# Kernel optimization log

Hardware: AMD Instinct MI355X
Metric: run time of the kernel (lower is better)

## Reference

```python
import jax, jax.numpy as jnp
import numpy as np

B = 2
M = 128
N = 128
D_EMBD = 512
N_HEADS = 8
D_HEAD = 64
S_WIN = 8
MW = M // S_WIN
NW = N // S_WIN
LEVELS = 3
S_REGION = [8, 6, 4]
S_POOL = [2, 2, 2]
THETA = 10000.0
POOLED = [(64, 64), (32, 32), (16, 16)]
RAD = THETA ** (-2.0 * jnp.arange(D_HEAD // 4, dtype=jnp.float32) / D_HEAD)


def rope(q, m_idx, n_idx):
    # 2D RoPE: first half of d_head rotated by row index, second half by col index
    m = m_idx.astype(jnp.float32)[:, None] * RAD  # (Lm, d_head//4)
    n = n_idx.astype(jnp.float32)[:, None] * RAD  # (Ln, d_head//4)
    cos_m, sin_m = jnp.cos(m)[:, None, :], jnp.sin(m)[:, None, :]
    cos_n, sin_n = jnp.cos(n)[None, :, :], jnp.sin(n)[None, :, :]
    d_half = D_HEAD // 2
    qm = q[..., :d_half].reshape(q.shape[:-1] + (d_half // 2, 2))
    qn = q[..., d_half:].reshape(q.shape[:-1] + (d_half // 2, 2))
    qm_rot = jnp.stack([cos_m * qm[..., 0] - sin_m * qm[..., 1],
                        sin_m * qm[..., 0] + cos_m * qm[..., 1]], axis=-1)
    qn_rot = jnp.stack([cos_n * qn[..., 0] - sin_n * qn[..., 1],
                        sin_n * qn[..., 0] + cos_n * qn[..., 1]], axis=-1)
    return jnp.concatenate([qm_rot.reshape(q.shape[:-1] + (d_half,)),
                            qn_rot.reshape(q.shape[:-1] + (d_half,))], axis=-1)


def extract_regions(X, cy, cx, k, pooled_mask):
    # X: (B,H,m,n,C), pooled_mask: (B,1,m,n,1). cy/cx mirror torch's in-place '+= pad'.
    b, h, m, n, c = X.shape
    pad = k // 2
    cy = cy + pad
    cx = cx + pad
    Xp = jnp.pad(X, ((0, 0), (0, 0), (pad, pad), (pad, pad), (0, 0)))
    mp = jnp.pad(pooled_mask, ((0, 0), (0, 0), (pad, pad), (pad, pad), (0, 0)))
    delta = jnp.arange(k) - k // 2
    YYg, XXg = jnp.meshgrid(cy, cx, indexing='ij')  # (Mw,Nw)
    YY = jnp.clip(YYg[..., None, None] + delta.reshape(1, 1, -1, 1), 0, m - 1)  # (Mw,Nw,k,1)
    XX = jnp.clip(XXg[..., None, None] + delta.reshape(1, 1, 1, -1), 0, n - 1)  # (Mw,Nw,1,k)
    regions = Xp[:, :, YY, XX, :]       # (B,H,Mw,Nw,k,k,C) broadcast gather
    mask_regions = mp[:, :, YY, XX, :]  # (B,1,Mw,Nw,k,k,1)
    mw, nw = YYg.shape
    regions = regions.transpose(0, 1, 2, 4, 3, 5, 6).reshape(b, h, mw * k, nw * k, c)
    mask_regions = mask_regions.reshape(mp.shape[0], 1, mw, nw, k * k, 1)
    return regions, mask_regions, YY - pad, XX - pad


def to_windows(x, s):
    # (B,h,Mw*s,Nw*s,d) -> (B,h,Mw,Nw,s*s,d)
    b, h, ms, ns, d = x.shape
    mw, nw = ms // s, ns // s
    return x.reshape(b, h, mw, s, nw, s, d).transpose(0, 1, 2, 4, 3, 5, 6).reshape(b, h, mw, nw, s * s, d)


def split_heads(x):
    b, m, n, _ = x.shape
    return x.reshape(b, m, n, N_HEADS, D_HEAD).transpose(0, 3, 1, 2, 4)


def forward(feature_map, pooled_map_0, pooled_map_1, pooled_map_2,
            pooled_mask_0, pooled_mask_1, pooled_mask_2,
            mask_q, freq_off, cy, cx, Wq, Wk, Wv, Wo):
    pooled_maps = [pooled_map_0, pooled_map_1, pooled_map_2]
    pooled_masks = [pooled_mask_0, pooled_mask_1, pooled_mask_2]
    Q = split_heads(feature_map @ Wq)           # (B,h,M,N,d)
    freq5 = freq_off[:, None]                   # (B,1,M,N,2*d_head)
    # query affine: M_grid/N_grid are identity arange gathers in the original code
    queries = Q * freq5[..., :D_HEAD] + freq5[..., D_HEAD:]
    queries = rope(queries, jnp.arange(M), jnp.arange(N))
    queries = to_windows(queries, S_WIN)        # (B,h,Mw,Nw,sw^2,d)
    mask_q5 = mask_q[:, None].astype(bool)      # (B,1,Mw,Nw,sw^2,1)

    K_list, V_list, maskK_list = [], [], []
    cy_run, cx_run = cy, cx
    for l in range(LEVELS):
        k = S_REGION[l]
        pad = k // 2
        Kl = split_heads(pooled_maps[l] @ Wk)
        Vl = split_heads(pooled_maps[l] @ Wv)
        pm5 = pooled_masks[l][:, None]          # (B,1,m,n,1)
        cy_run = cy_run // S_POOL[l]
        cx_run = cx_run // S_POOL[l]
        K_reg, mask_K, YY, XX = extract_regions(Kl, cy_run, cx_run, k, pm5)
        # torch extract_regions mutates cy/cx in place (+pad), so V sees shifted centers
        V_reg, _, _, _ = extract_regions(Vl, cy_run + pad, cx_run + pad, k, pm5)
        cy_run = cy_run + 2 * pad
        cx_run = cx_run + 2 * pad
        m_idx = jnp.clip(YY[:, 0, :, 0].reshape(-1) * S_POOL[l], 0, M - 1)  # (Mw*k,)
        n_idx = jnp.clip(XX[0, :, 0, :].reshape(-1) * S_POOL[l], 0, N - 1)  # (Nw*k,)
        fgl = freq5[:, :, m_idx[:, None], n_idx[None, :], :]  # (B,1,Mw*k,Nw*k,2d)
        K_reg = rope(K_reg * fgl[..., :D_HEAD] + fgl[..., D_HEAD:], m_idx, n_idx)
        V_reg = rope(V_reg * fgl[..., :D_HEAD] + fgl[..., D_HEAD:], m_idx, n_idx)
        K_list.append(to_windows(K_reg, k))
        V_list.append(to_windows(V_reg, k))
        maskK_list.append(mask_K)
    keys = jnp.concatenate(K_list, axis=-2)     # (B,h,Mw,Nw,S,d), S=sum(sr^2)=116
    vals = jnp.concatenate(V_list, axis=-2)
    mask_keys = jnp.concatenate(maskK_list, axis=-2)  # (B,1,Mw,Nw,S,1)
    attn_mask = mask_q5 & jnp.swapaxes(mask_keys, -1, -2).astype(bool)
    scores = jnp.einsum('bhmnqd,bhmnkd->bhmnqk', queries, keys) / jnp.sqrt(jnp.float32(D_HEAD))
    scores = jnp.where(attn_mask, scores, jnp.finfo(scores.dtype).min)
    att = jnp.einsum('bhmnqk,bhmnkd->bhmnqd', jax.nn.softmax(scores, axis=-1), vals)
    att = att.reshape(B, N_HEADS, MW, NW, S_WIN, S_WIN, D_HEAD)
    att = att.transpose(0, 2, 4, 3, 5, 1, 6).reshape(B, M, N, N_HEADS * D_HEAD)
    return att @ Wo


def setup_inputs():
    key = jax.random.key(0)
    ks = jax.random.split(key, 12)
    inp = {}
    inp['feature_map'] = jax.random.normal(ks[0], (B, M, N, D_EMBD), dtype=jnp.float32)
    for l in range(LEVELS):
        m, n = POOLED[l]
        inp['pooled_map_%d' % l] = jax.random.normal(ks[1 + l], (B, m, n, D_EMBD), dtype=jnp.float32)
        inp['pooled_mask_%d' % l] = jnp.ones((B, m, n, 1), dtype=jnp.float32)
    inp['mask_q'] = jnp.ones((B, MW, NW, S_WIN * S_WIN, 1), dtype=bool)
    inp['freq_off'] = jax.random.normal(ks[4], (B, M, N, 2 * D_HEAD), dtype=jnp.float32) * 0.1 + 1.0
    inp['cy'] = (jnp.arange(MW) * S_WIN + S_WIN // 2).astype(jnp.int32)
    inp['cx'] = (jnp.arange(NW) * S_WIN + S_WIN // 2).astype(jnp.int32)
    inp['Wq'] = jax.random.normal(ks[5], (D_EMBD, N_HEADS * D_HEAD), dtype=jnp.float32) / np.sqrt(D_EMBD)
    inp['Wk'] = jax.random.normal(ks[6], (D_EMBD, N_HEADS * D_HEAD), dtype=jnp.float32) / np.sqrt(D_EMBD)
    inp['Wv'] = jax.random.normal(ks[7], (D_EMBD, N_HEADS * D_HEAD), dtype=jnp.float32) / np.sqrt(D_EMBD)
    inp['Wo'] = jax.random.normal(ks[8], (N_HEADS * D_HEAD, D_EMBD), dtype=jnp.float32) / np.sqrt(N_HEADS * D_HEAD)
    return inp


def reference(feature_map, pooled_map_0, pooled_map_1, pooled_map_2,
              pooled_mask_0, pooled_mask_1, pooled_mask_2,
              mask_q, freq_off, cy, cx, Wq, Wk, Wv, Wo):
    return forward(feature_map, pooled_map_0, pooled_map_1, pooled_map_2,
                   pooled_mask_0, pooled_mask_1, pooled_mask_2,
                   mask_q, freq_off, cy, cx, Wq, Wk, Wv, Wo)
```

## Files before the change

### kernel.cpp

```cpp
#include <hip/hip_runtime.h>
#include <math.h>

#define BB 2
#define MM 128
#define NN 128
#define DE 512
#define NH 8
#define DH 64
#define SWIN 8
#define MWIN 16
#define NWIN 16
#define NKEY 116
#define NSLOT 128

#define NEG_MAX (-3.402823466e38f)
#define LN1E4_OVER_32 0.28782313662425575f

#define L0_BASE 0
#define L1_BASE 8192
#define L2_BASE 10240
#define NPOS_KV 10752

typedef __bf16 bf16_t;
typedef bf16_t bf16x8 __attribute__((ext_vector_type(8)));
typedef bf16_t bf16x4 __attribute__((ext_vector_type(4)));
typedef bf16_t bf16x2 __attribute__((ext_vector_type(2)));
typedef float  f32x4  __attribute__((ext_vector_type(4)));

#define CV_S0 16777216
#define CV_S1 20971520
#define CV_S2 22020096
#define CV_S3 22282240
#define CV_BLOCKS 21760
__global__ __launch_bounds__(256) void prep(
    const float* __restrict__ fmap, const float* __restrict__ p0,
    const float* __restrict__ p1, const float* __restrict__ p2,
    const float* __restrict__ Wq, const float* __restrict__ Wk,
    const float* __restrict__ Wv, const float* __restrict__ Wo,
    bf16_t* __restrict__ Afm, bf16_t* __restrict__ Ap0,
    bf16_t* __restrict__ Ap1, bf16_t* __restrict__ Ap2,
    bf16_t* __restrict__ Tq, bf16_t* __restrict__ Tk,
    bf16_t* __restrict__ Tv, bf16_t* __restrict__ To) {
    __shared__ float Ws[64][65];
    const int bid = blockIdx.x;
    const int tid = threadIdx.x;
    if (bid < CV_BLOCKS) {
        const int e = (bid * 256 + tid) * 4;
        const float* src; bf16_t* dst; int off;
        if (e < CV_S0)      { src = fmap; dst = Afm; off = e; }
        else if (e < CV_S1) { src = p0;   dst = Ap0; off = e - CV_S0; }
        else if (e < CV_S2) { src = p1;   dst = Ap1; off = e - CV_S1; }
        else if (e < CV_S3) { src = p2;   dst = Ap2; off = e - CV_S2; }
        else return;
        const float4 v = *(const float4*)(src + off);
        bf16x4 o;
        o[0] = (bf16_t)v.x; o[1] = (bf16_t)v.y; o[2] = (bf16_t)v.z; o[3] = (bf16_t)v.w;
        *(bf16x4*)(dst + off) = o;
    } else {
        const int idx = bid - CV_BLOCKS;
        const int w = idx >> 6, tile = idx & 63;
        const float* W = (w == 0) ? Wq : (w == 1) ? Wk : (w == 2) ? Wv : Wo;
        bf16_t*      T = (w == 0) ? Tq : (w == 1) ? Tk : (w == 2) ? Tv : To;
        const int tk0 = (tile >> 3) * 64;
        const int tn0 = (tile & 7) * 64;
#pragma unroll 4
        for (int i = 0; i < 16; ++i) {
            const int e = tid + i * 256;
            Ws[e >> 6][e & 63] = W[(tk0 + (e >> 6)) * 512 + tn0 + (e & 63)];
        }
        __syncthreads();
#pragma unroll 4
        for (int i = 0; i < 16; ++i) {
            const int e = tid + i * 256;
            const int ck = e & 63, rn = e >> 6;
            T[(size_t)(tn0 + rn) * 512 + tk0 + ck] = (bf16_t)Ws[ck][rn];
        }
    }
}

__device__ __forceinline__ void gemm_body(const bf16_t* __restrict__ A,
                                          const bf16_t* __restrict__ Bt,
                                          float* __restrict__ C,
                                          int row0, int col0) {
    __shared__ __align__(16) bf16_t sA[128][72];
    __shared__ __align__(16) bf16_t sB[128][72];
    const int tid  = threadIdx.x;
    const int wave = tid >> 6;
    const int lane = tid & 63;
    const int quad = lane >> 4;
    const int lr   = lane & 15;
    const int m_w  = (wave >> 1) * 64;
    const int n_w  = (wave & 1) * 64;

    f32x4 acc[4][4];
#pragma unroll
    for (int i = 0; i < 4; ++i)
#pragma unroll
        for (int j = 0; j < 4; ++j)
#pragma unroll
            for (int r = 0; r < 4; ++r) acc[i][j][r] = 0.0f;

    for (int k0 = 0; k0 < 512; k0 += 64) {
#pragma unroll
        for (int i = 0; i < 4; ++i) {
            const int c  = tid + i * 256;
            const int r  = c >> 3;
            const int cb = (c & 7) * 8;
            *(bf16x8*)&sA[r][cb] = *(const bf16x8*)(A  + (size_t)(row0 + r) * 512 + k0 + cb);
            *(bf16x8*)&sB[r][cb] = *(const bf16x8*)(Bt + (size_t)(col0 + r) * 512 + k0 + cb);
        }
        __syncthreads();
#pragma unroll
        for (int kk = 0; kk < 64; kk += 32) {
            bf16x8 af[4], bfr[4];
#pragma unroll
            for (int i = 0; i < 4; ++i)
                af[i] = *(const bf16x8*)&sA[m_w + i * 16 + lr][kk + quad * 8];
#pragma unroll
            for (int j = 0; j < 4; ++j)
                bfr[j] = *(const bf16x8*)&sB[n_w + j * 16 + lr][kk + quad * 8];
#pragma unroll
            for (int i = 0; i < 4; ++i)
#pragma unroll
                for (int j = 0; j < 4; ++j)
                    acc[i][j] = __builtin_amdgcn_mfma_f32_16x16x32_bf16(
                        af[i], bfr[j], acc[i][j], 0, 0, 0);
        }
        __syncthreads();
    }
#pragma unroll
    for (int i = 0; i < 4; ++i) {
        const int rb = row0 + m_w + i * 16 + quad * 4;
#pragma unroll
        for (int j = 0; j < 4; ++j) {
            const int col = col0 + n_w + j * 16 + lr;
#pragma unroll
            for (int r = 0; r < 4; ++r)
                C[(size_t)(rb + r) * 512 + col] = acc[i][j][r];
        }
    }
}

__global__ __launch_bounds__(256) void gemm_all(
    const bf16_t* __restrict__ Afm, const bf16_t* __restrict__ Ap0,
    const bf16_t* __restrict__ Ap1, const bf16_t* __restrict__ Ap2,
    const bf16_t* __restrict__ Tq, const bf16_t* __restrict__ Tk,
    const bf16_t* __restrict__ Tv,
    float* __restrict__ Qbuf, float* __restrict__ K0, float* __restrict__ V0,
    float* __restrict__ K1, float* __restrict__ V1,
    float* __restrict__ K2, float* __restrict__ V2) {
    const int t = blockIdx.x;
    const bf16_t* A; const bf16_t* Bt; float* C; int rt;
    if (t < 1024)      { A = Afm; Bt = Tq; C = Qbuf; rt = t >> 2; }
    else if (t < 1280) { A = Ap0; Bt = Tk; C = K0; rt = (t - 1024) >> 2; }
    else if (t < 1536) { A = Ap0; Bt = Tv; C = V0; rt = (t - 1280) >> 2; }
    else if (t < 1600) { A = Ap1; Bt = Tk; C = K1; rt = (t - 1536) >> 2; }
    else if (t < 1664) { A = Ap1; Bt = Tv; C = V1; rt = (t - 1600) >> 2; }
    else if (t < 1680) { A = Ap2; Bt = Tk; C = K2; rt = (t - 1664) >> 2; }
    else               { A = Ap2; Bt = Tv; C = V2; rt = (t - 1680) >> 2; }
    gemm_body(A, Bt, C, rt * 128, (t & 3) * 128);
}

__global__ __launch_bounds__(256) void gemm_out(const bf16_t* __restrict__ A,
                                                const bf16_t* __restrict__ Bt,
                                                float* __restrict__ C) {
    gemm_body(A, Bt, C, blockIdx.y * 128, blockIdx.x * 128);
}

__global__ __launch_bounds__(256) void rope_qb(const float* __restrict__ Q,
                                               const float* __restrict__ freq,
                                               bf16_t* __restrict__ Qb) {
    const int t   = blockIdx.x * 256 + threadIdx.x;
    const int pp  = t & 255;
    const int pos = t >> 8;
    const int n   = pos & 127;
    const int m   = (pos >> 7) & 127;
    const int h   = pp >> 5;
    const int pr  = pp & 31;
    const int p   = pr & 15;
    const int d0  = (pr < 16) ? (2 * p) : (32 + 2 * p);

    const float rad   = expf(-LN1E4_OVER_32 * (float)p);
    const float angle = (float)((pr < 16) ? m : n) * rad;
    float sn, cs;
    sincosf(angle, &sn, &cs);

    const size_t fb = (size_t)pos * 128;
    const size_t qb = (size_t)pos * 512 + h * 64;
    const float x0 = Q[qb + d0]     * freq[fb + d0]     + freq[fb + 64 + d0];
    const float x1 = Q[qb + d0 + 1] * freq[fb + d0 + 1] + freq[fb + 64 + d0 + 1];
    bf16x2 o;
    o[0] = (bf16_t)(cs * x0 - sn * x1);
    o[1] = (bf16_t)(sn * x0 + cs * x1);
    *(bf16x2*)(Qb + qb + d0) = o;
}

__global__ __launch_bounds__(256) void rope_kv(
    const float* __restrict__ K0, const float* __restrict__ K1, const float* __restrict__ K2,
    const float* __restrict__ V0, const float* __restrict__ V1, const float* __restrict__ V2,
    const float* __restrict__ freq,
    bf16_t* __restrict__ RK, bf16_t* __restrict__ RV) {
    const int pos = blockIdx.x;
    int l, ml, pad, rel;
    if (pos < L1_BASE)      { l = 0; ml = 64; pad = 4; rel = pos; }
    else if (pos < L2_BASE) { l = 1; ml = 32; pad = 3; rel = pos - L1_BASE; }
    else                    { l = 2; ml = 16; pad = 2; rel = pos - L2_BASE; }
    const int b  = rel / (ml * ml);
    const int yx = rel - b * ml * ml;
    const int y  = yx / ml, x = yx % ml;
    const int vy = min(y + pad, ml - 1 - pad);
    const int vx = min(x + pad, ml - 1 - pad);
    const int mi = min(2 * y, 127), ni = min(2 * x, 127);
    const float* Kl = (l == 0) ? K0 : (l == 1) ? K1 : K2;
    const float* Vl = (l == 0) ? V0 : (l == 1) ? V1 : V2;

    const int tid = threadIdx.x;
    const int h  = tid >> 5;
    const int pr = tid & 31;
    const int p  = pr & 15;
    const int d0 = (pr < 16) ? (2 * p) : (32 + 2 * p);
    const float rad = expf(-LN1E4_OVER_32 * (float)p);
    const float ang = (float)((pr < 16) ? mi : ni) * rad;
    float sn, cs;
    sincosf(ang, &sn, &cs);

    const size_t fb   = ((size_t)(b * 128 + mi) * 128 + ni) * 128;
    const float fs0 = freq[fb + d0],      fs1 = freq[fb + d0 + 1];
    const float fo0 = freq[fb + 64 + d0], fo1 = freq[fb + 64 + d0 + 1];
    const size_t kidx = ((size_t)(b * ml + y) * ml + x) * 512 + h * 64 + d0;
    const size_t vidx = ((size_t)(b * ml + vy) * ml + vx) * 512 + h * 64 + d0;
    const size_t oidx = (size_t)pos * 512 + h * 64 + d0;
    {
        const float x0 = Kl[kidx] * fs0 + fo0, x1 = Kl[kidx + 1] * fs1 + fo1;
        bf16x2 o;
        o[0] = (bf16_t)(cs * x0 - sn * x1);
        o[1] = (bf16_t)(sn * x0 + cs * x1);
        *(bf16x2*)(RK + oidx) = o;
    }
    {
        const float x0 = Vl[vidx] * fs0 + fo0, x1 = Vl[vidx + 1] * fs1 + fo1;
        bf16x2 o;
        o[0] = (bf16_t)(cs * x0 - sn * x1);
        o[1] = (bf16_t)(sn * x0 + cs * x1);
        *(bf16x2*)(RV + oidx) = o;
    }
}

#define SKS 72
#define SPS 136
#define SVS 134
__global__ __launch_bounds__(256, 4) void attn_mfma(
    const bf16_t* __restrict__ Qb,
    const bf16_t* __restrict__ RK, const bf16_t* __restrict__ RV,
    const float* __restrict__ pm0, const float* __restrict__ pm1, const float* __restrict__ pm2,
    const int* __restrict__ cy, const int* __restrict__ cx,
    bf16_t* __restrict__ att) {
    __shared__ __align__(16) bf16_t sK[NSLOT * SKS];
    __shared__ __align__(16) bf16_t sVt[64 * SVS];
    __shared__ int   sOff[NSLOT];
    __shared__ float sValid[NSLOT];
    bf16_t* sP = sK;

    const int tid = threadIdx.x;
    const int h  = blockIdx.x & 7;
    const int wx = (blockIdx.x >> 3) & 15;
    const int wy = (blockIdx.x >> 7) & 15;
    const int b  = blockIdx.x >> 11;

    const int wave = tid >> 6, lane = tid & 63, quad = lane >> 4, lr = lane & 15;

    const int qrow = wave * 16 + lr;
    const int mq0 = wy * 8 + (qrow >> 3), nq0 = wx * 8 + (qrow & 7);
    const bf16_t* qp = Qb + ((size_t)((b * 128 + mq0) * 128 + nq0)) * 512 + h * 64 + quad * 8;
    const bf16x8 af0 = *(const bf16x8*)qp;
    const bf16x8 af1 = *(const bf16x8*)(qp + 32);

    if (tid < NSLOT) {
        const int j = tid;
        int off = 0;
        bool valid = false;
        if (j < NKEY) {
            const int c0y = cy[wy] >> 1, c0x = cx[wx] >> 1;
            const int c1y = (c0y + 8) >> 1, c1x = (c0x + 8) >> 1;
            const int c2y = (c1y + 6) >> 1, c2x = (c1x + 6) >> 1;
            int dy, dx, cry, crx, ml, pad, lbase;
            if (j < 64)       { dy = j >> 3;           dx = j & 7;  cry = c0y; crx = c0x; ml = 64; pad = 4; lbase = L0_BASE; }
            else if (j < 100) { int u = j - 64;  dy = u / 6;  dx = u % 6; cry = c1y; crx = c1x; ml = 32; pad = 3; lbase = L1_BASE; }
            else              { int u = j - 100; dy = u >> 2; dx = u & 3; cry = c2y; crx = c2x; ml = 16; pad = 2; lbase = L2_BASE; }
            const int ky = min(cry + dy, ml - 1) - pad;
            const int kx = min(crx + dx, ml - 1) - pad;
            if (ky >= 0 && kx >= 0) {
                const float* pm = (j < 64) ? pm0 : (j < 100) ? pm1 : pm2;
                valid = (pm[(b * ml + ky) * ml + kx] != 0.0f);
            }
            off = (lbase + (b * ml + max(ky, 0)) * ml + max(kx, 0)) * 512 + h * 64;
        }
        sOff[tid]   = off;
        sValid[tid] = valid ? 1.0f : 0.0f;
    }
    __syncthreads();

#pragma unroll
    for (int it = 0; it < 4; ++it) {
        const int idx = tid + it * 256;
        const int j = idx >> 3, c = (idx & 7) * 8;
        const int off = sOff[j];
        *(bf16x8*)&sK[j * SKS + c] = *(const bf16x8*)(RK + off + c);
        const bf16x8 v = *(const bf16x8*)(RV + off + c);
#pragma unroll
        for (int e = 0; e < 8; ++e) sVt[(c + e) * SVS + j] = v[e];
    }
    __syncthreads();

    f32x4 accs[8];
#pragma unroll
    for (int nt = 0; nt < 8; ++nt)
#pragma unroll
        for (int r = 0; r < 4; ++r) accs[nt][r] = 0.0f;
#pragma unroll
    for (int nt = 0; nt < 8; ++nt) {
        const bf16x8 b0 = *(const bf16x8*)&sK[(nt * 16 + lr) * SKS + quad * 8];
        const bf16x8 b1 = *(const bf16x8*)&sK[(nt * 16 + lr) * SKS + quad * 8 + 32];
        accs[nt] = __builtin_amdgcn_mfma_f32_16x16x32_bf16(af0, b0, accs[nt], 0, 0, 0);
        accs[nt] = __builtin_amdgcn_mfma_f32_16x16x32_bf16(af1, b1, accs[nt], 0, 0, 0);
    }

    float P[8][4];
#pragma unroll
    for (int nt = 0; nt < 8; ++nt) {
        const float vf = sValid[nt * 16 + lr];
#pragma unroll
        for (int r = 0; r < 4; ++r)
            P[nt][r] = (vf != 0.0f) ? accs[nt][r] * 0.125f : NEG_MAX;
    }

#pragma unroll
    for (int r = 0; r < 4; ++r) {
        float mx = P[0][r];
#pragma unroll
        for (int nt = 1; nt < 8; ++nt) mx = fmaxf(mx, P[nt][r]);
        for (int m = 1; m < 16; m <<= 1) mx = fmaxf(mx, __shfl_xor(mx, m));
        float sum = 0.0f;
#pragma unroll
        for (int nt = 0; nt < 8; ++nt) {
            const float e = __expf(P[nt][r] - mx);
            P[nt][r] = e;
            sum += e;
        }
        for (int m = 1; m < 16; m <<= 1) sum += __shfl_xor(sum, m);
        const float inv = 1.0f / sum;
#pragma unroll
        for (int nt = 0; nt < 8; ++nt) P[nt][r] *= inv;
    }

    __syncthreads();

#pragma unroll
    for (int nt = 0; nt < 8; ++nt)
#pragma unroll
        for (int r = 0; r < 4; ++r)
            sP[(wave * 16 + quad * 4 + r) * SPS + nt * 16 + lr] = (bf16_t)P[nt][r];
    __syncthreads();

    f32x4 acco[4];
#pragma unroll
    for (int nt = 0; nt < 4; ++nt)
#pragma unroll
        for (int r = 0; r < 4; ++r) acco[nt][r] = 0.0f;

    bf16x8 pa[4];
#pragma unroll
    for (int ks = 0; ks < 4; ++ks)
        pa[ks] = *(const bf16x8*)&sP[(wave * 16 + lr) * SPS + quad * 8 + ks * 32];
#pragma unroll
    for (int nt = 0; nt < 4; ++nt) {
#pragma unroll
        for (int ks = 0; ks < 4; ++ks) {
            const bf16x8 vb = *(const bf16x8*)&sVt[(nt * 16 + lr) * SVS + quad * 8 + ks * 32];
            acco[nt] = __builtin_amdgcn_mfma_f32_16x16x32_bf16(pa[ks], vb, acco[nt], 0, 0, 0);
        }
    }

#pragma unroll
    for (int nt = 0; nt < 4; ++nt) {
#pragma unroll
        for (int r = 0; r < 4; ++r) {
            const int q  = wave * 16 + quad * 4 + r;
            const int d  = nt * 16 + lr;
            const int mq = wy * 8 + (q >> 3), nq = wx * 8 + (q & 7);
            att[((size_t)((b * 128 + mq) * 128 + nq)) * 512 + h * 64 + d] = (bf16_t)acco[nt][r];
        }
    }
}

extern "C" void kernel_launch(void* const* d_in, const int* in_sizes, int n_in,
                              void* d_out, int out_size, void* d_ws, size_t ws_size,
                              hipStream_t stream) {
    const float* fmap = (const float*)d_in[0];
    const float* p0   = (const float*)d_in[1];
    const float* pm0  = (const float*)d_in[2];
    const float* p1   = (const float*)d_in[3];
    const float* pm1  = (const float*)d_in[4];
    const float* p2   = (const float*)d_in[5];
    const float* pm2  = (const float*)d_in[6];
    const float* freq = (const float*)d_in[8];
    const int*   cy   = (const int*)d_in[9];
    const int*   cx   = (const int*)d_in[10];
    const float* Wq   = (const float*)d_in[11];
    const float* Wk   = (const float*)d_in[12];
    const float* Wv   = (const float*)d_in[13];
    const float* Wo   = (const float*)d_in[14];
    float* out = (float*)d_out;

    char* base = (char*)d_ws;
    size_t off = 0;
    auto carve = [&](size_t bytes) {
        char* p = base + off; off += (bytes + 255) & ~(size_t)255; return p;
    };
    float*  Qbuf = (float*)carve(67108864);
    float*  K0   = (float*)carve(16777216);
    float*  V0   = (float*)carve(16777216);
    float*  K1   = (float*)carve(4194304);
    float*  K2   = (float*)carve(1048576);
    float*  V1   = (float*)carve(4194304);
    float*  V2   = (float*)carve(1048576);
    bf16_t* Afm  = (bf16_t*)carve(33554432);
    bf16_t* Ap0  = (bf16_t*)carve(8388608);
    bf16_t* Ap1  = (bf16_t*)carve(2097152);
    bf16_t* Ap2  = (bf16_t*)carve(524288);
    bf16_t* Tq   = (bf16_t*)carve(524288);
    bf16_t* Tk   = (bf16_t*)carve(524288);
    bf16_t* Tv   = (bf16_t*)carve(524288);
    bf16_t* To   = (bf16_t*)carve(524288);
    bf16_t* Qbf  = Afm;
    bf16_t* RK   = (bf16_t*)Qbuf;
    bf16_t* RV   = RK + (size_t)NPOS_KV * 512;
    bf16_t* attb = (bf16_t*)K0;

    prep<<<CV_BLOCKS + 256, 256, 0, stream>>>(fmap, p0, p1, p2, Wq, Wk, Wv, Wo,
                                              Afm, Ap0, Ap1, Ap2, Tq, Tk, Tv, To);

    gemm_all<<<1696, 256, 0, stream>>>(Afm, Ap0, Ap1, Ap2, Tq, Tk, Tv,
                                       Qbuf, K0, V0, K1, V1, K2, V2);

    rope_qb<<<BB * MM * NN, 256, 0, stream>>>(Qbuf, freq, Qbf);

    rope_kv<<<NPOS_KV, 256, 0, stream>>>(K0, K1, K2, V0, V1, V2, freq, RK, RV);

    attn_mfma<<<BB * MWIN * NWIN * NH, 256, 0, stream>>>(Qbf, RK, RV,
                                                         pm0, pm1, pm2, cy, cx, attb);

    gemm_out<<<dim3(4, 256), 256, 0, stream>>>(attb, To, out);
}
```

Measured before the change: 334.2 us.

## Fuse Q RoPE into projection GEMM epilogue and store K/V projections as bf16

The Q projection GEMM now applies the frequency scale/offset and 2D RoPE rotation in its epilogue and writes bf16 directly, which removes the separate rope_qb kernel and the fp32 Q round trip through memory. K/V projections are written as bf16 instead of fp32, halving intermediate traffic, and rope_kv reads bf16. Block-to-tile mapping is also reordered so consecutive blocks share a column tile. The cost is extra sincos work and shuffles in the GEMM epilogue, plus an extra bf16 rounding before the K/V RoPE.

```diff
diff --git a/kernel.cpp b/kernel.cpp
--- a/kernel.cpp
+++ b/kernel.cpp
@@ -78,12 +78,14 @@
     }
 }
 
-__device__ __forceinline__ void gemm_body(const bf16_t* __restrict__ A,
+template <int MODE>
+__device__ __forceinline__ void gemm_body(bf16_t* __restrict__ sA,
+                                          bf16_t* __restrict__ sB,
+                                          const bf16_t* __restrict__ A,
                                           const bf16_t* __restrict__ Bt,
-                                          float* __restrict__ C,
-                                          int row0, int col0) {
-    __shared__ __align__(16) bf16_t sA[128][72];
-    __shared__ __align__(16) bf16_t sB[128][72];
+                                          void* __restrict__ Cp,
+                                          int row0, int col0,
+                                          const float* __restrict__ freq) {
     const int tid  = threadIdx.x;
     const int wave = tid >> 6;
     const int lane = tid & 63;
@@ -106,8 +108,8 @@
             const int c  = tid + i * 256;
             const int r  = c >> 3;
             const int cb = (c & 7) * 8;
-            *(bf16x8*)&sA[r][cb] = *(const bf16x8*)(A  + (size_t)(row0 + r) * 512 + k0 + cb);
-            *(bf16x8*)&sB[r][cb] = *(const bf16x8*)(Bt + (size_t)(col0 + r) * 512 + k0 + cb);
+            *(bf16x8*)&sA[r * 72 + cb] = *(const bf16x8*)(A  + (size_t)(row0 + r) * 512 + k0 + cb);
+            *(bf16x8*)&sB[r * 72 + cb] = *(const bf16x8*)(Bt + (size_t)(col0 + r) * 512 + k0 + cb);
         }
         __syncthreads();
 #pragma unroll
@@ -115,10 +117,10 @@
             bf16x8 af[4], bfr[4];
 #pragma unroll
             for (int i = 0; i < 4; ++i)
-                af[i] = *(const bf16x8*)&sA[m_w + i * 16 + lr][kk + quad * 8];
+                af[i] = *(const bf16x8*)&sA[(m_w + i * 16 + lr) * 72 + kk + quad * 8];
 #pragma unroll
             for (int j = 0; j < 4; ++j)
-                bfr[j] = *(const bf16x8*)&sB[n_w + j * 16 + lr][kk + quad * 8];
+                bfr[j] = *(const bf16x8*)&sB[(n_w + j * 16 + lr) * 72 + kk + quad * 8];
 #pragma unroll
             for (int i = 0; i < 4; ++i)
 #pragma unroll
@@ -128,15 +130,65 @@
         }
         __syncthreads();
     }
-#pragma unroll
-    for (int i = 0; i < 4; ++i) {
-        const int rb = row0 + m_w + i * 16 + quad * 4;
-#pragma unroll
-        for (int j = 0; j < 4; ++j) {
-            const int col = col0 + n_w + j * 16 + lr;
-#pragma unroll
-            for (int r = 0; r < 4; ++r)
-                C[(size_t)(rb + r) * 512 + col] = acc[i][j][r];
+
+    if (MODE == 0) {
+        float* C = (float*)Cp;
+#pragma unroll
+        for (int i = 0; i < 4; ++i) {
+            const int rb = row0 + m_w + i * 16 + quad * 4;
+#pragma unroll
+            for (int j = 0; j < 4; ++j) {
+                const int col = col0 + n_w + j * 16 + lr;
+#pragma unroll
+                for (int r = 0; r < 4; ++r)
+                    C[(size_t)(rb + r) * 512 + col] = acc[i][j][r];
+            }
+        }
+    } else if (MODE == 2) {
+        bf16_t* C = (bf16_t*)Cp;
+#pragma unroll
+        for (int i = 0; i < 4; ++i) {
+            const int rb = row0 + m_w + i * 16 + quad * 4;
+#pragma unroll
+            for (int j = 0; j < 4; ++j) {
+                const int col = col0 + n_w + j * 16 + lr;
+#pragma unroll
+                for (int r = 0; r < 4; ++r)
+                    C[(size_t)(rb + r) * 512 + col] = (bf16_t)acc[i][j][r];
+            }
+        }
+    } else {
+        bf16_t* C = (bf16_t*)Cp;
+        const int mbase = (row0 >> 7) & 127;
+        const float rad0 = expf(-LN1E4_OVER_32 * (float)(lr >> 1));
+        const float rad1 = expf(-LN1E4_OVER_32 * (float)(8 + (lr >> 1)));
+        float cs_m[2], sn_m[2];
+        sincosf((float)mbase * rad0, &sn_m[0], &cs_m[0]);
+        sincosf((float)mbase * rad1, &sn_m[1], &cs_m[1]);
+#pragma unroll
+        for (int i = 0; i < 4; ++i) {
+#pragma unroll
+            for (int r = 0; r < 4; ++r) {
+                const int rr = m_w + i * 16 + quad * 4 + r;
+                const size_t pos = (size_t)row0 + rr;
+                float sn_n[2], cs_n[2];
+                sincosf((float)rr * rad0, &sn_n[0], &cs_n[0]);
+                sincosf((float)rr * rad1, &sn_n[1], &cs_n[1]);
+                const float* fq = freq + pos * 128;
+#pragma unroll
+                for (int j = 0; j < 4; ++j) {
+                    const int col = col0 + n_w + j * 16 + lr;
+                    const int d   = j * 16 + lr;
+                    const float fs = fq[d], fo = fq[64 + d];
+                    const float xp = acc[i][j][r] * fs + fo;
+                    const float pr = __shfl_xor(xp, 1);
+                    const float cs = (j < 2) ? cs_m[j & 1] : cs_n[j & 1];
+                    const float sn = (j < 2) ? sn_m[j & 1] : sn_n[j & 1];
+                    const float o  = (lr & 1) ? (sn * pr + cs * xp)
+                                              : (cs * xp - sn * pr);
+                    C[pos * 512 + col] = (bf16_t)o;
+                }
+            }
         }
     }
 }
@@ -146,58 +198,49 @@
     const bf16_t* __restrict__ Ap1, const bf16_t* __restrict__ Ap2,
     const bf16_t* __restrict__ Tq, const bf16_t* __restrict__ Tk,
     const bf16_t* __restrict__ Tv,
-    float* __restrict__ Qbuf, float* __restrict__ K0, float* __restrict__ V0,
-    float* __restrict__ K1, float* __restrict__ V1,
-    float* __restrict__ K2, float* __restrict__ V2) {
+    bf16_t* __restrict__ Qbf,
+    bf16_t* __restrict__ K0, bf16_t* __restrict__ V0,
+    bf16_t* __restrict__ K1, bf16_t* __restrict__ V1,
+    bf16_t* __restrict__ K2, bf16_t* __restrict__ V2,
+    const float* __restrict__ freq) {
+    __shared__ __align__(16) bf16_t sA[128 * 72];
+    __shared__ __align__(16) bf16_t sB[128 * 72];
     const int t = blockIdx.x;
-    const bf16_t* A; const bf16_t* Bt; float* C; int rt;
-    if (t < 1024)      { A = Afm; Bt = Tq; C = Qbuf; rt = t >> 2; }
-    else if (t < 1280) { A = Ap0; Bt = Tk; C = K0; rt = (t - 1024) >> 2; }
-    else if (t < 1536) { A = Ap0; Bt = Tv; C = V0; rt = (t - 1280) >> 2; }
-    else if (t < 1600) { A = Ap1; Bt = Tk; C = K1; rt = (t - 1536) >> 2; }
-    else if (t < 1664) { A = Ap1; Bt = Tv; C = V1; rt = (t - 1600) >> 2; }
-    else if (t < 1680) { A = Ap2; Bt = Tk; C = K2; rt = (t - 1664) >> 2; }
-    else               { A = Ap2; Bt = Tv; C = V2; rt = (t - 1680) >> 2; }
-    gemm_body(A, Bt, C, rt * 128, (t & 3) * 128);
+    if (t < 1024) {
+        gemm_body<1>(sA, sB, Afm, Tq, Qbf, (t & 255) * 128, (t >> 8) * 128, freq);
+    } else if (t < 1280) {
+        const int u = t - 1024;
+        gemm_body<2>(sA, sB, Ap0, Tk, K0, (u & 63) * 128, (u >> 6) * 128, nullptr);
+    } else if (t < 1536) {
+        const int u = t - 1280;
+        gemm_body<2>(sA, sB, Ap0, Tv, V0, (u & 63) * 128, (u >> 6) * 128, nullptr);
+    } else if (t < 1600) {
+        const int u = t - 1536;
+        gemm_body<2>(sA, sB, Ap1, Tk, K1, (u & 15) * 128, (u >> 4) * 128, nullptr);
+    } else if (t < 1664) {
+        const int u = t - 1600;
+        gemm_body<2>(sA, sB, Ap1, Tv, V1, (u & 15) * 128, (u >> 4) * 128, nullptr);
+    } else if (t < 1680) {
+        const int u = t - 1664;
+        gemm_body<2>(sA, sB, Ap2, Tk, K2, (u & 3) * 128, (u >> 2) * 128, nullptr);
+    } else {
+        const int u = t - 1680;
+        gemm_body<2>(sA, sB, Ap2, Tv, V2, (u & 3) * 128, (u >> 2) * 128, nullptr);
+    }
 }
 
 __global__ __launch_bounds__(256) void gemm_out(const bf16_t* __restrict__ A,
                                                 const bf16_t* __restrict__ Bt,
                                                 float* __restrict__ C) {
-    gemm_body(A, Bt, C, blockIdx.y * 128, blockIdx.x * 128);
-}
-
-__global__ __launch_bounds__(256) void rope_qb(const float* __restrict__ Q,
-                                               const float* __restrict__ freq,
-                                               bf16_t* __restrict__ Qb) {
-    const int t   = blockIdx.x * 256 + threadIdx.x;
-    const int pp  = t & 255;
-    const int pos = t >> 8;
-    const int n   = pos & 127;
-    const int m   = (pos >> 7) & 127;
-    const int h   = pp >> 5;
-    const int pr  = pp & 31;
-    const int p   = pr & 15;
-    const int d0  = (pr < 16) ? (2 * p) : (32 + 2 * p);
-
-    const float rad   = expf(-LN1E4_OVER_32 * (float)p);
-    const float angle = (float)((pr < 16) ? m : n) * rad;
-    float sn, cs;
-    sincosf(angle, &sn, &cs);
-
-    const size_t fb = (size_t)pos * 128;
-    const size_t qb = (size_t)pos * 512 + h * 64;
-    const float x0 = Q[qb + d0]     * freq[fb + d0]     + freq[fb + 64 + d0];
-    const float x1 = Q[qb + d0 + 1] * freq[fb + d0 + 1] + freq[fb + 64 + d0 + 1];
-    bf16x2 o;
-    o[0] = (bf16_t)(cs * x0 - sn * x1);
-    o[1] = (bf16_t)(sn * x0 + cs * x1);
-    *(bf16x2*)(Qb + qb + d0) = o;
+    __shared__ __align__(16) bf16_t sA[128 * 72];
+    __shared__ __align__(16) bf16_t sB[128 * 72];
+    const int t = blockIdx.x;
+    gemm_body<0>(sA, sB, A, Bt, C, (t & 255) * 128, (t >> 8) * 128, nullptr);
 }
 
 __global__ __launch_bounds__(256) void rope_kv(
-    const float* __restrict__ K0, const float* __restrict__ K1, const float* __restrict__ K2,
-    const float* __restrict__ V0, const float* __restrict__ V1, const float* __restrict__ V2,
+    const bf16_t* __restrict__ K0, const bf16_t* __restrict__ K1, const bf16_t* __restrict__ K2,
+    const bf16_t* __restrict__ V0, const bf16_t* __restrict__ V1, const bf16_t* __restrict__ V2,
     const float* __restrict__ freq,
     bf16_t* __restrict__ RK, bf16_t* __restrict__ RV) {
     const int pos = blockIdx.x;
@@ -211,8 +254,8 @@
     const int vy = min(y + pad, ml - 1 - pad);
     const int vx = min(x + pad, ml - 1 - pad);
     const int mi = min(2 * y, 127), ni = min(2 * x, 127);
-    const float* Kl = (l == 0) ? K0 : (l == 1) ? K1 : K2;
-    const float* Vl = (l == 0) ? V0 : (l == 1) ? V1 : V2;
+    const bf16_t* Kl = (l == 0) ? K0 : (l == 1) ? K1 : K2;
+    const bf16_t* Vl = (l == 0) ? V0 : (l == 1) ? V1 : V2;
 
     const int tid = threadIdx.x;
     const int h  = tid >> 5;
@@ -231,14 +274,16 @@
     const size_t vidx = ((size_t)(b * ml + vy) * ml + vx) * 512 + h * 64 + d0;
     const size_t oidx = (size_t)pos * 512 + h * 64 + d0;
     {
-        const float x0 = Kl[kidx] * fs0 + fo0, x1 = Kl[kidx + 1] * fs1 + fo1;
+        const float x0 = (float)Kl[kidx] * fs0 + fo0;
+        const float x1 = (float)Kl[kidx + 1] * fs1 + fo1;
         bf16x2 o;
         o[0] = (bf16_t)(cs * x0 - sn * x1);
         o[1] = (bf16_t)(sn * x0 + cs * x1);
         *(bf16x2*)(RK + oidx) = o;
     }
     {
-        const float x0 = Vl[vidx] * fs0 + fo0, x1 = Vl[vidx + 1] * fs1 + fo1;
+        const float x0 = (float)Vl[vidx] * fs0 + fo0;
+        const float x1 = (float)Vl[vidx + 1] * fs1 + fo1;
         bf16x2 o;
         o[0] = (bf16_t)(cs * x0 - sn * x1);
         o[1] = (bf16_t)(sn * x0 + cs * x1);
@@ -417,13 +462,6 @@
     auto carve = [&](size_t bytes) {
         char* p = base + off; off += (bytes + 255) & ~(size_t)255; return p;
     };
-    float*  Qbuf = (float*)carve(67108864);
-    float*  K0   = (float*)carve(16777216);
-    float*  V0   = (float*)carve(16777216);
-    float*  K1   = (float*)carve(4194304);
-    float*  K2   = (float*)carve(1048576);
-    float*  V1   = (float*)carve(4194304);
-    float*  V2   = (float*)carve(1048576);
     bf16_t* Afm  = (bf16_t*)carve(33554432);
     bf16_t* Ap0  = (bf16_t*)carve(8388608);
     bf16_t* Ap1  = (bf16_t*)carve(2097152);
@@ -432,23 +470,27 @@
     bf16_t* Tk   = (bf16_t*)carve(524288);
     bf16_t* Tv   = (bf16_t*)carve(524288);
     bf16_t* To   = (bf16_t*)carve(524288);
-    bf16_t* Qbf  = Afm;
-    bf16_t* RK   = (bf16_t*)Qbuf;
-    bf16_t* RV   = RK + (size_t)NPOS_KV * 512;
-    bf16_t* attb = (bf16_t*)K0;
+    bf16_t* Qbf  = (bf16_t*)carve(33554432);
+    bf16_t* K0   = (bf16_t*)carve(8388608);
+    bf16_t* V0   = (bf16_t*)carve(8388608);
+    bf16_t* K1   = (bf16_t*)carve(2097152);
+    bf16_t* V1   = (bf16_t*)carve(2097152);
+    bf16_t* K2   = (bf16_t*)carve(524288);
+    bf16_t* V2   = (bf16_t*)carve(524288);
+    bf16_t* RK   = (bf16_t*)carve(11010048);
+    bf16_t* RV   = (bf16_t*)carve(11010048);
+    bf16_t* attb = Afm;
 
     prep<<<CV_BLOCKS + 256, 256, 0, stream>>>(fmap, p0, p1, p2, Wq, Wk, Wv, Wo,
                                               Afm, Ap0, Ap1, Ap2, Tq, Tk, Tv, To);
 
     gemm_all<<<1696, 256, 0, stream>>>(Afm, Ap0, Ap1, Ap2, Tq, Tk, Tv,
-                                       Qbuf, K0, V0, K1, V1, K2, V2);
-
-    rope_qb<<<BB * MM * NN, 256, 0, stream>>>(Qbuf, freq, Qbf);
+                                       Qbf, K0, V0, K1, V1, K2, V2, freq);
 
     rope_kv<<<NPOS_KV, 256, 0, stream>>>(K0, K1, K2, V0, V1, V2, freq, RK, RV);
 
     attn_mfma<<<BB * MWIN * NWIN * NH, 256, 0, stream>>>(Qbf, RK, RV,
                                                          pm0, pm1, pm2, cy, cx, attb);
 
-    gemm_out<<<dim3(4, 256), 256, 0, stream>>>(attb, To, out);
-}
+    gemm_out<<<1024, 256, 0, stream>>>(attb, To, out);
+}
```

Result: faster. 327.2 us (-2.1%).
